# Kernel tuning notes

Hardware: AMD Instinct MI355X
Metric: run time of the kernel (lower is better)

## Reference

```python
import jax, jax.numpy as jnp
import numpy as np

N_NODES = 100000
N_EDGES = 1600000
NFEAT, NHID1, NCLASS = 256, 128, 64
NUM_GRAPHS = 64


def gcn_conv(x, edge_index, edge_weight, W, b):
    # PyG GCNConv: linear transform, add self-loops (weight 1), symmetric norm, scatter-add
    n = x.shape[0]
    x = x @ W  # [N, out]
    loop = jnp.arange(n)
    row = jnp.concatenate([edge_index[0], loop])  # source
    col = jnp.concatenate([edge_index[1], loop])  # target
    w = jnp.concatenate([edge_weight, jnp.ones((n,), dtype=x.dtype)])
    deg = jax.ops.segment_sum(w, col, num_segments=n)
    dinv = jnp.where(deg > 0, jax.lax.rsqrt(jnp.maximum(deg, 1e-30)), 0.0)
    norm = dinv[row] * w * dinv[col]  # [E+N]
    out = jax.ops.segment_sum(x[row] * norm[:, None], col, num_segments=n)
    return out + b


def setup_inputs() -> dict:
    key = jax.random.key(0)
    ks = jax.random.split(key, 12)
    x = jax.random.normal(ks[0], (N_NODES, NFEAT), dtype=jnp.float32)
    edge_index = jax.random.randint(ks[1], (2, N_EDGES), 0, N_NODES, dtype=jnp.int64)
    edge_weight = jax.random.uniform(ks[2], (N_EDGES,), dtype=jnp.float32)
    batch = jnp.sort(jax.random.randint(ks[3], (N_NODES,), 0, NUM_GRAPHS, dtype=jnp.int64))
    def glorot(k, shape):
        lim = float(np.sqrt(6.0 / (shape[0] + shape[1])))
        return jax.random.uniform(k, shape, jnp.float32, -lim, lim)
    W1 = glorot(ks[4], (NFEAT, NHID1)); b1 = jnp.zeros((NHID1,), jnp.float32)
    W2 = glorot(ks[5], (NHID1, NCLASS)); b2 = jnp.zeros((NCLASS,), jnp.float32)
    l1w = glorot(ks[6], (NCLASS, 64)); l1b = jnp.zeros((64,), jnp.float32)
    l2w = glorot(ks[7], (64, 2)); l2b = jnp.zeros((2,), jnp.float32)
    return {"x": x, "edge_index": edge_index, "edge_weight": edge_weight, "batch": batch,
            "W1": W1, "b1": b1, "W2": W2, "b2": b2,
            "l1w": l1w, "l1b": l1b, "l2w": l2w, "l2b": l2b}


def reference(x, edge_index, edge_weight, batch, W1, b1, W2, b2, l1w, l1b, l2w, l2b):
    h = jax.nn.relu(gcn_conv(x, edge_index, edge_weight, W1, b1))
    h = jax.nn.relu(gcn_conv(h, edge_index, edge_weight, W2, b2))
    pooled = jax.ops.segment_sum(h, batch, num_segments=NUM_GRAPHS)  # global_add_pool
    h = jax.nn.relu(pooled @ l1w + l1b)
    out = h @ l2w + l2b
    Y_prob = jax.nn.log_softmax(out, axis=1)
    Y_hat = jnp.argmax(Y_prob, axis=1).astype(jnp.float32)
    return (Y_prob, Y_hat, out)
```

## Files before the change

### kernel.cpp

```cpp
#include <hip/hip_runtime.h>
#include <hip/hip_bf16.h>
#include <math.h>

#define N_NODES 100000
#define N_EDGES 1600000
#define NFEAT 256
#define NHID1 128
#define NCLASS 64
#define NUM_GRAPHS 64

#define NBUCK 391
#define EPB 8192
#define NBLK_A 196

typedef __attribute__((ext_vector_type(8))) short bf16x8;
typedef __attribute__((ext_vector_type(4))) float f32x4;
typedef __attribute__((ext_vector_type(4))) unsigned u32x4;


__device__ __forceinline__ unsigned short f2bf(float f) {
    unsigned u = __float_as_uint(f);
    u += 0x7fffu + ((u >> 16) & 1u);
    return (unsigned short)(u >> 16);
}
__device__ __forceinline__ unsigned packbf2(float lo, float hi) {
    return (unsigned)f2bf(lo) | ((unsigned)f2bf(hi) << 16);
}
__device__ __forceinline__ float bflo(unsigned p) { return __uint_as_float(p << 16); }
__device__ __forceinline__ float bfhi(unsigned p) { return __uint_as_float(p & 0xffff0000u); }


__global__ __launch_bounds__(256) void hist_kernel(const int* __restrict__ cols,
                                                   int* __restrict__ ghist, int nE) {
    __shared__ int h[NBUCK];
    const int tid = threadIdx.x;
    for (int i = tid; i < NBUCK; i += 256) h[i] = 0;
    __syncthreads();
    long base = (long)blockIdx.x * EPB;
    for (int j = tid; j < EPB; j += 256) {
        long idx = base + j;
        if (idx < nE) atomicAdd(&h[cols[idx] >> 8], 1);
    }
    __syncthreads();
    for (int i = tid; i < NBUCK; i += 256) {
        int v = h[i];
        if (v) atomicAdd(&ghist[i], v);
    }
}


__global__ __launch_bounds__(512) void bucket_scan_kernel(const int* __restrict__ ghist,
                                                          int* __restrict__ gbase,
                                                          int* __restrict__ gcursor) {
    __shared__ int sh[512];
    int t = threadIdx.x;
    int v = (t < NBUCK) ? ghist[t] : 0;
    sh[t] = v;
    __syncthreads();
    for (int off = 1; off < 512; off <<= 1) {
        int add = (t >= off) ? sh[t - off] : 0;
        __syncthreads();
        sh[t] += add;
        __syncthreads();
    }
    if (t < NBUCK) {
        int excl = sh[t] - v;
        gbase[t] = excl;
        gcursor[t] = excl;
    }
}


__global__ __launch_bounds__(256) void scatter_bucket_kernel(const int* __restrict__ rows,
                                                             const int* __restrict__ cols,
                                                             const float* __restrict__ w,
                                                             int* __restrict__ gcursor,
                                                             int2* __restrict__ csc_tmp, int nE) {
    __shared__ int h[NBUCK];
    __shared__ int bb[NBUCK];
    __shared__ unsigned short rk[EPB];
    const int tid = threadIdx.x;
    for (int i = tid; i < NBUCK; i += 256) h[i] = 0;
    __syncthreads();
    long base = (long)blockIdx.x * EPB;
    for (int j = tid; j < EPB; j += 256) {
        long idx = base + j;
        if (idx < nE) rk[j] = (unsigned short)atomicAdd(&h[cols[idx] >> 8], 1);
    }
    __syncthreads();
    for (int i = tid; i < NBUCK; i += 256) {
        int v = h[i];
        if (v) bb[i] = atomicAdd(&gcursor[i], v);
    }
    __syncthreads();
    for (int j = tid; j < EPB; j += 256) {
        long idx = base + j;
        if (idx < nE) {
            int c = cols[idx];
            int b = c >> 8;
            int pos = bb[b] + (int)rk[j];
            csc_tmp[pos] = make_int2((rows[idx] & 0x1FFFF) | ((c & 255) << 17),
                                     __float_as_int(w[idx]));
        }
    }
}


__global__ __launch_bounds__(256) void build_csc_kernel(const int2* __restrict__ csc_tmp,
                                                        const int* __restrict__ gbase,
                                                        const int* __restrict__ ghist,
                                                        int2* __restrict__ edges,
                                                        int* __restrict__ starts,
                                                        int* __restrict__ cnt,
                                                        float* __restrict__ dinv, int n) {
    __shared__ int ncnt[256];
    __shared__ float nws[256];
    __shared__ int sh[256];
    __shared__ int ncur[256];
    const int tid = threadIdx.x;
    const int b = blockIdx.x;
    const int base = gbase[b];
    const int cntb = ghist[b];

    ncnt[tid] = 0;
    nws[tid] = 0.f;
    __syncthreads();

    for (int i = tid; i < cntb; i += 256) {
        int2 rec = csc_tmp[base + i];
        int local = ((unsigned)rec.x) >> 17;
        atomicAdd(&ncnt[local], 1);
        atomicAdd(&nws[local], __int_as_float(rec.y));
    }
    __syncthreads();

    int v = ncnt[tid];
    sh[tid] = v;
    __syncthreads();
    for (int off = 1; off < 256; off <<= 1) {
        int add = (tid >= off) ? sh[tid - off] : 0;
        __syncthreads();
        sh[tid] += add;
        __syncthreads();
    }
    int excl = sh[tid] - v;
    ncur[tid] = excl;

    int node = (b << 8) + tid;
    if (node < n) {
        cnt[node] = v;
        starts[node] = base + excl;
        dinv[node] = rsqrtf(1.0f + nws[tid]);
    }
    __syncthreads();

    for (int i = tid; i < cntb; i += 256) {
        int2 rec = csc_tmp[base + i];
        int local = ((unsigned)rec.x) >> 17;
        int r = rec.x & 0x1FFFF;
        int pos = base + atomicAdd(&ncur[local], 1);
        edges[pos] = make_int2(r, rec.y);
    }
}


__global__ void transpose_bf_kernel(const float* __restrict__ W, unsigned* __restrict__ WT,
                                    int K, int Nn) {
    int idx = blockIdx.x * blockDim.x + threadIdx.x;
    int total = Nn * (K / 2);
    if (idx < total) {
        int n = idx / (K / 2);
        int kp = idx - n * (K / 2);
        WT[idx] = packbf2(W[(2 * kp) * Nn + n], W[(2 * kp + 1) * Nn + n]);
    }
}


template <int NT, int KK, bool ABF16>
__global__ __launch_bounds__(256) void gemm_mfma(const void* __restrict__ Av,
                                                 const unsigned* __restrict__ BT,
                                                 const float* __restrict__ rowscale,
                                                 unsigned short* __restrict__ C,
                                                 int M) {
    constexpr int CT = NT / 16;
    constexpr int KD = KK / 2;
    __shared__ unsigned Al[4][128][4];
    __shared__ unsigned Bl[4][NT][4];
    const int tid = threadIdx.x;
    const int wave = tid >> 6;
    const int lane = tid & 63;
    const int quad = lane >> 4;
    const int l16 = lane & 15;
    const int row0 = blockIdx.x * 128;

    f32x4 acc[2][CT] = {};

    for (int k0 = 0; k0 < KK; k0 += 32) {
        if (ABF16) {
            const unsigned* Ab = (const unsigned*)Av;
            #pragma unroll
            for (int i = 0; i < 2; i++) {
                int idx = tid + i * 256;
                int ar = idx >> 2, aq = idx & 3;
                uint4 v = make_uint4(0, 0, 0, 0);
                if (row0 + ar < M)
                    v = *(const uint4*)(Ab + (long)(row0 + ar) * KD + k0 / 2 + aq * 4);
                *(uint4*)&Al[aq][ar][0] = v;
            }
        } else {
            const float* Af = (const float*)Av;
            int ar = tid >> 1, ah = tid & 1;
            float4 v0 = make_float4(0, 0, 0, 0), v1 = v0, v2 = v0, v3 = v0;
            if (row0 + ar < M) {
                const float* p = Af + (long)(row0 + ar) * KK + k0 + ah * 16;
                v0 = *(const float4*)p;
                v1 = *(const float4*)(p + 4);
                v2 = *(const float4*)(p + 8);
                v3 = *(const float4*)(p + 12);
            }
            uint4 d0 = make_uint4(packbf2(v0.x, v0.y), packbf2(v0.z, v0.w),
                                  packbf2(v1.x, v1.y), packbf2(v1.z, v1.w));
            uint4 d1 = make_uint4(packbf2(v2.x, v2.y), packbf2(v2.z, v2.w),
                                  packbf2(v3.x, v3.y), packbf2(v3.z, v3.w));
            *(uint4*)&Al[ah * 2 + 0][ar][0] = d0;
            *(uint4*)&Al[ah * 2 + 1][ar][0] = d1;
        }
        #pragma unroll
        for (int i = 0; i < NT / 64; i++) {
            int idx = tid + i * 256;
            int br = idx >> 2, bq = idx & 3;
            *(uint4*)&Bl[bq][br][0] = *(const uint4*)(BT + (long)br * KD + k0 / 2 + bq * 4);
        }
        __syncthreads();

        bf16x8 af[2];
        #pragma unroll
        for (int rt = 0; rt < 2; rt++)
            af[rt] = *(const bf16x8*)&Al[quad][wave * 32 + rt * 16 + l16][0];
        #pragma unroll
        for (int ct = 0; ct < CT; ct++) {
            bf16x8 bfr = *(const bf16x8*)&Bl[quad][ct * 16 + l16][0];
            acc[0][ct] = __builtin_amdgcn_mfma_f32_16x16x32_bf16(af[0], bfr, acc[0][ct], 0, 0, 0);
            acc[1][ct] = __builtin_amdgcn_mfma_f32_16x16x32_bf16(af[1], bfr, acc[1][ct], 0, 0, 0);
        }
        __syncthreads();
    }

    #pragma unroll
    for (int rt = 0; rt < 2; rt++) {
        #pragma unroll
        for (int reg = 0; reg < 4; reg++) {
            int row = row0 + wave * 32 + rt * 16 + quad * 4 + reg;
            if (row < M) {
                float sc = rowscale[row];
                unsigned short* cp = C + (long)row * NT + l16;
                #pragma unroll
                for (int ct = 0; ct < CT; ct++)
                    cp[ct * 16] = f2bf(acc[rt][ct][reg] * sc);
            }
        }
    }
}


template <int F, bool RELU, int OUTMODE>
__global__ __launch_bounds__(256) void gather_agg_bf(const unsigned* __restrict__ xsb,
                                                     const int2* __restrict__ edges,
                                                     const int* __restrict__ starts,
                                                     const int* __restrict__ cnt,
                                                     const float* __restrict__ dinv,
                                                     const float* __restrict__ bias,
                                                     const int* __restrict__ batch,
                                                     void* __restrict__ outv, int n) {
    constexpr int G = F / 8;
    constexpr int FU = F / 2;
    int gt = blockIdx.x * blockDim.x + threadIdx.x;
    int node = gt / G;
    int lane = gt - node * G;

    if (OUTMODE != 2 && node >= n) return;
    bool active = (node < n);

    __shared__ float lp[4][64];
    int g0 = 0;
    if (OUTMODE == 2) {
        lp[threadIdx.x >> 6][threadIdx.x & 63] = 0.f;
        int firstnode = (blockIdx.x * blockDim.x) / G;
        if (firstnode >= n) firstnode = n - 1;
        g0 = batch[firstnode];
        __syncthreads();
    }

    float acc[8] = {};
    float d = 0.f;
    const unsigned* lbase = xsb + lane * 4;

    if (active) {
        int s = starts[node];
        int c = cnt[node];
        int e = s + c;

        int j = s;
        for (; j + 3 < e; j += 4) {
            long long q0 = __builtin_nontemporal_load((const long long*)(edges + j));
            long long q1 = __builtin_nontemporal_load((const long long*)(edges + j + 1));
            long long q2 = __builtin_nontemporal_load((const long long*)(edges + j + 2));
            long long q3 = __builtin_nontemporal_load((const long long*)(edges + j + 3));
            int r0 = (int)q0, r1 = (int)q1, r2 = (int)q2, r3 = (int)q3;
            float w0 = __int_as_float((int)(q0 >> 32));
            float w1 = __int_as_float((int)(q1 >> 32));
            float w2 = __int_as_float((int)(q2 >> 32));
            float w3 = __int_as_float((int)(q3 >> 32));
            uint4 p0 = *(const uint4*)(lbase + (long)r0 * FU);
            uint4 p1 = *(const uint4*)(lbase + (long)r1 * FU);
            uint4 p2 = *(const uint4*)(lbase + (long)r2 * FU);
            uint4 p3 = *(const uint4*)(lbase + (long)r3 * FU);
            acc[0] += bflo(p0.x) * w0; acc[1] += bfhi(p0.x) * w0;
            acc[2] += bflo(p0.y) * w0; acc[3] += bfhi(p0.y) * w0;
            acc[4] += bflo(p0.z) * w0; acc[5] += bfhi(p0.z) * w0;
            acc[6] += bflo(p0.w) * w0; acc[7] += bfhi(p0.w) * w0;
            acc[0] += bflo(p1.x) * w1; acc[1] += bfhi(p1.x) * w1;
            acc[2] += bflo(p1.y) * w1; acc[3] += bfhi(p1.y) * w1;
            acc[4] += bflo(p1.z) * w1; acc[5] += bfhi(p1.z) * w1;
            acc[6] += bflo(p1.w) * w1; acc[7] += bfhi(p1.w) * w1;
            acc[0] += bflo(p2.x) * w2; acc[1] += bfhi(p2.x) * w2;
            acc[2] += bflo(p2.y) * w2; acc[3] += bfhi(p2.y) * w2;
            acc[4] += bflo(p2.z) * w2; acc[5] += bfhi(p2.z) * w2;
            acc[6] += bflo(p2.w) * w2; acc[7] += bfhi(p2.w) * w2;
            acc[0] += bflo(p3.x) * w3; acc[1] += bfhi(p3.x) * w3;
            acc[2] += bflo(p3.y) * w3; acc[3] += bfhi(p3.y) * w3;
            acc[4] += bflo(p3.z) * w3; acc[5] += bfhi(p3.z) * w3;
            acc[6] += bflo(p3.w) * w3; acc[7] += bfhi(p3.w) * w3;
        }
        for (; j < e; j++) {
            long long q = __builtin_nontemporal_load((const long long*)(edges + j));
            int r = (int)q;
            float wv = __int_as_float((int)(q >> 32));
            uint4 p = *(const uint4*)(lbase + (long)r * FU);
            acc[0] += bflo(p.x) * wv; acc[1] += bfhi(p.x) * wv;
            acc[2] += bflo(p.y) * wv; acc[3] += bfhi(p.y) * wv;
            acc[4] += bflo(p.z) * wv; acc[5] += bfhi(p.z) * wv;
            acc[6] += bflo(p.w) * wv; acc[7] += bfhi(p.w) * wv;
        }
        d = dinv[node];
    }

    float r[8] = {};
    if (active) {
        uint4 sp = *(const uint4*)(lbase + (long)node * FU);
        float sv[8] = { bflo(sp.x), bfhi(sp.x), bflo(sp.y), bfhi(sp.y),
                        bflo(sp.z), bfhi(sp.z), bflo(sp.w), bfhi(sp.w) };
        float4 bb0 = ((const float4*)bias)[lane * 2];
        float4 bb1 = ((const float4*)bias)[lane * 2 + 1];
        float bbv[8] = { bb0.x, bb0.y, bb0.z, bb0.w, bb1.x, bb1.y, bb1.z, bb1.w };
        #pragma unroll
        for (int i = 0; i < 8; i++) {
            float v = d * (acc[i] + sv[i]) + bbv[i];
            r[i] = RELU ? fmaxf(v, 0.f) : v;
        }
    }

    if (OUTMODE == 1) {
        if (active) {
            unsigned* ob = (unsigned*)outv;
            u32x4 pk = { packbf2(r[0], r[1]), packbf2(r[2], r[3]),
                         packbf2(r[4], r[5]), packbf2(r[6], r[7]) };
            __builtin_nontemporal_store(pk, (u32x4*)(ob + (long)node * FU + lane * 4));
        }
    } else if (OUTMODE == 0) {
        if (active) {
            float* o = (float*)outv + (long)node * F + lane * 8;
            *(float4*)o       = make_float4(r[0], r[1], r[2], r[3]);
            *(float4*)(o + 4) = make_float4(r[4], r[5], r[6], r[7]);
        }
    } else {
        float* pooled = (float*)outv;
        if (active) {
            int g = batch[node];
            int rel = g - g0;
            if (rel >= 0 && rel < 4) {
                #pragma unroll
                for (int i = 0; i < 8; i++)
                    atomicAdd(&lp[rel][lane * 8 + i], r[i]);
            } else {
                #pragma unroll
                for (int i = 0; i < 8; i++)
                    atomicAdd(&pooled[g * 64 + lane * 8 + i], r[i]);
            }
        }
        __syncthreads();
        int idx = threadIdx.x;
        int rel = idx >> 6, feat = idx & 63;
        float v = lp[rel][feat];
        int g = g0 + rel;
        if (v != 0.f && g < NUM_GRAPHS)
            atomicAdd(&pooled[g * 64 + feat], v);
    }
}


__global__ __launch_bounds__(256) void head_kernel(const float* __restrict__ pooled,
                                                   const float* __restrict__ l1w,
                                                   const float* __restrict__ l1b,
                                                   const float* __restrict__ l2w,
                                                   const float* __restrict__ l2b,
                                                   float* __restrict__ out) {
    __shared__ float P[64][68];
    __shared__ float W[64][68];
    __shared__ float red0[64][4];
    __shared__ float red1[64][4];
    const int tid = threadIdx.x;

    for (int i = tid; i < 1024; i += 256) {
        int r = i >> 4;
        int cq = (i & 15) * 4;
        *(float4*)&P[r][cq] = *(const float4*)&pooled[r * 64 + cq];
        *(float4*)&W[r][cq] = *(const float4*)&l1w[r * 64 + cq];
    }
    __syncthreads();

    const int g = tid >> 2;
    const int q = tid & 3;
    const int j0 = q * 16;

    float hacc[16];
    #pragma unroll
    for (int jj = 0; jj < 16; jj++) hacc[jj] = l1b[j0 + jj];

    for (int c = 0; c < 64; c++) {
        float pv = P[g][c];
        #pragma unroll
        for (int jj = 0; jj < 16; jj += 4) {
            float4 wv = *(const float4*)&W[c][j0 + jj];
            hacc[jj + 0] += pv * wv.x;
            hacc[jj + 1] += pv * wv.y;
            hacc[jj + 2] += pv * wv.z;
            hacc[jj + 3] += pv * wv.w;
        }
    }

    float o0 = 0.f, o1 = 0.f;
    #pragma unroll
    for (int jj = 0; jj < 16; jj++) {
        float h = fmaxf(hacc[jj], 0.f);
        o0 += h * l2w[(j0 + jj) * 2];
        o1 += h * l2w[(j0 + jj) * 2 + 1];
    }
    red0[g][q] = o0;
    red1[g][q] = o1;
    __syncthreads();

    if (q == 0) {
        float a0 = red0[g][0] + red0[g][1] + red0[g][2] + red0[g][3] + l2b[0];
        float a1 = red1[g][0] + red1[g][1] + red1[g][2] + red1[g][3] + l2b[1];
        float m = fmaxf(a0, a1);
        float lse = m + logf(expf(a0 - m) + expf(a1 - m));
        out[g * 2 + 0] = a0 - lse;
        out[g * 2 + 1] = a1 - lse;
        out[128 + g] = (a1 > a0) ? 1.f : 0.f;
        out[192 + g * 2 + 0] = a0;
        out[192 + g * 2 + 1] = a1;
    }
}


extern "C" void kernel_launch(void* const* d_in, const int* in_sizes, int n_in,
                              void* d_out, int out_size, void* d_ws, size_t ws_size,
                              hipStream_t stream) {
    const float* x   = (const float*)d_in[0];
    const int* eidx  = (const int*)d_in[1];
    const float* ew  = (const float*)d_in[2];
    const int* batch = (const int*)d_in[3];
    const float* W1  = (const float*)d_in[4];
    const float* b1  = (const float*)d_in[5];
    const float* W2  = (const float*)d_in[6];
    const float* b2  = (const float*)d_in[7];
    const float* l1w = (const float*)d_in[8];
    const float* l1b = (const float*)d_in[9];
    const float* l2w = (const float*)d_in[10];
    const float* l2b = (const float*)d_in[11];
    float* out = (float*)d_out;

    const int N = N_NODES, E = N_EDGES;
    const int* rows = eidx;
    const int* cols = eidx + E;

    float* ws = (float*)d_ws;
    int*   ghist   = (int*)ws;
    int*   gbase   = ghist + 512;
    int*   gcursor = gbase + 512;
    float* dinv    = (float*)(gcursor + 512);
    int*   cnt     = (int*)(dinv + N);
    int*   starts  = cnt + N;
    unsigned* w1t  = (unsigned*)(starts + N);
    unsigned* w2t  = w1t + 16384;
    int2*  csc_tmp = (int2*)(w2t + 4096);
    int2*  edges   = csc_tmp + E;
    unsigned* xsb  = (unsigned*)(edges + E);
    unsigned* h1b  = xsb + (long)N * 64;
    float* pooled  = (float*)(h1b + (long)N * 64);
    unsigned* hw2b = xsb;

    hipMemsetAsync(ghist, 0, 512 * sizeof(int), stream);
    hist_kernel<<<NBLK_A, 256, 0, stream>>>(cols, ghist, E);

    bucket_scan_kernel<<<1, 512, 0, stream>>>(ghist, gbase, gcursor);

    scatter_bucket_kernel<<<NBLK_A, 256, 0, stream>>>(rows, cols, ew, gcursor, csc_tmp, E);

    build_csc_kernel<<<NBUCK, 256, 0, stream>>>(csc_tmp, gbase, ghist, edges, starts, cnt, dinv, N);

    transpose_bf_kernel<<<64, 256, 0, stream>>>(W1, w1t, NFEAT, NHID1);
    transpose_bf_kernel<<<16, 256, 0, stream>>>(W2, w2t, NHID1, NCLASS);

    gemm_mfma<NHID1, NFEAT, false><<<(N + 127) / 128, 256, 0, stream>>>(
        x, w1t, dinv, (unsigned short*)xsb, N);

    {
        long threads = (long)N * (NHID1 / 8);
        gather_agg_bf<NHID1, true, 1><<<(threads + 255) / 256, 256, 0, stream>>>(
            xsb, edges, starts, cnt, dinv, b1, batch, h1b, N);
    }

    gemm_mfma<NCLASS, NHID1, true><<<(N + 127) / 128, 256, 0, stream>>>(
        h1b, w2t, dinv, (unsigned short*)hw2b, N);

    hipMemsetAsync(pooled, 0, NUM_GRAPHS * NCLASS * sizeof(float), stream);
    {
        long threads = (long)N * (NCLASS / 8);
        gather_agg_bf<NCLASS, true, 2><<<(threads + 255) / 256, 256, 0, stream>>>(
            hw2b, edges, starts, cnt, dinv, b2, batch, pooled, N);
    }

    head_kernel<<<1, 256, 0, stream>>>(pooled, l1w, l1b, l2w, l2b, out);
}
```

Before: 436.4 us.

## Restructure GEMM to stream A from registers, stage C via LDS, merge transposes

The GEMM now loads A fragments straight from global memory into registers and stages half of B in LDS per pass. This removes the per-32-K-step LDS round trip and the paired barriers. Output tiles are written into LDS first and then stored with coalesced 16-byte writes instead of scattered 2-byte stores. The two weight-transpose launches are merged into one kernel, and the gather kernel drops its nontemporal loads and stores in favour of plain accesses. In exchange, A rows are read with less coalescing, and LDS use and register pressure rise.

```diff
diff --git a/kernel.cpp b/kernel.cpp
--- a/kernel.cpp
+++ b/kernel.cpp
@@ -15,7 +15,6 @@
 
 typedef __attribute__((ext_vector_type(8))) short bf16x8;
 typedef __attribute__((ext_vector_type(4))) float f32x4;
-typedef __attribute__((ext_vector_type(4))) unsigned u32x4;
 
 
 __device__ __forceinline__ unsigned short f2bf(float f) {
@@ -164,14 +163,16 @@
 }
 
 
-__global__ void transpose_bf_kernel(const float* __restrict__ W, unsigned* __restrict__ WT,
-                                    int K, int Nn) {
+__global__ void transpose2_kernel(const float* __restrict__ W1, unsigned* __restrict__ W1T,
+                                  const float* __restrict__ W2, unsigned* __restrict__ W2T) {
     int idx = blockIdx.x * blockDim.x + threadIdx.x;
-    int total = Nn * (K / 2);
-    if (idx < total) {
-        int n = idx / (K / 2);
-        int kp = idx - n * (K / 2);
-        WT[idx] = packbf2(W[(2 * kp) * Nn + n], W[(2 * kp + 1) * Nn + n]);
+    if (idx < 16384) {
+        int n = idx >> 7, kp = idx & 127;
+        W1T[idx] = packbf2(W1[(2 * kp) * NHID1 + n], W1[(2 * kp + 1) * NHID1 + n]);
+    } else if (idx < 16384 + 4096) {
+        int i2 = idx - 16384;
+        int n = i2 >> 6, kp = i2 & 63;
+        W2T[i2] = packbf2(W2[(2 * kp) * NCLASS + n], W2[(2 * kp + 1) * NCLASS + n]);
     }
 }
 
@@ -184,80 +185,95 @@
                                                  int M) {
     constexpr int CT = NT / 16;
     constexpr int KD = KK / 2;
-    __shared__ unsigned Al[4][128][4];
-    __shared__ unsigned Bl[4][NT][4];
+    constexpr int BHP = KD / 2 + 4;
+    constexpr int BSZ = NT * BHP * 4;
+    constexpr int CPITCH = NT + 8;
+    constexpr int CSZ = 128 * CPITCH * 2;
+    constexpr int SMEM = (BSZ > CSZ) ? BSZ : CSZ;
+    __shared__ __align__(16) unsigned char smem[SMEM];
+    unsigned* Bl = reinterpret_cast<unsigned*>(smem);
+    unsigned short* Cl = reinterpret_cast<unsigned short*>(smem);
+
     const int tid = threadIdx.x;
     const int wave = tid >> 6;
     const int lane = tid & 63;
     const int quad = lane >> 4;
     const int l16 = lane & 15;
     const int row0 = blockIdx.x * 128;
+    const int arow0 = row0 + wave * 32 + l16;
 
     f32x4 acc[2][CT] = {};
 
-    for (int k0 = 0; k0 < KK; k0 += 32) {
-        if (ABF16) {
-            const unsigned* Ab = (const unsigned*)Av;
+    #pragma unroll
+    for (int h = 0; h < 2; h++) {
+        if (h) __syncthreads();
+        for (int i = tid; i < NT * (KD / 8); i += 256) {
+            int br = i / (KD / 8);
+            int bq = i - br * (KD / 8);
+            *(uint4*)&Bl[br * BHP + bq * 4] =
+                *(const uint4*)(BT + (long)br * KD + h * (KD / 2) + bq * 4);
+        }
+        __syncthreads();
+
+        #pragma unroll
+        for (int kl = 0; kl < KK / 64; kl++) {
+            const int ki = h * (KK / 64) + kl;
+            bf16x8 af[2];
             #pragma unroll
-            for (int i = 0; i < 2; i++) {
-                int idx = tid + i * 256;
-                int ar = idx >> 2, aq = idx & 3;
+            for (int rt = 0; rt < 2; rt++) {
+                int r = arow0 + rt * 16;
                 uint4 v = make_uint4(0, 0, 0, 0);
-                if (row0 + ar < M)
-                    v = *(const uint4*)(Ab + (long)(row0 + ar) * KD + k0 / 2 + aq * 4);
-                *(uint4*)&Al[aq][ar][0] = v;
+                if (ABF16) {
+                    const unsigned* Ab = (const unsigned*)Av;
+                    if (r < M)
+                        v = *(const uint4*)(Ab + (long)r * KD + ki * 16 + quad * 4);
+                } else {
+                    const float* Af = (const float*)Av;
+                    float4 a0 = make_float4(0, 0, 0, 0), a1 = a0;
+                    if (r < M) {
+                        const float* p = Af + (long)r * KK + ki * 32 + quad * 8;
+                        a0 = *(const float4*)p;
+                        a1 = *(const float4*)(p + 4);
+                    }
+                    v = make_uint4(packbf2(a0.x, a0.y), packbf2(a0.z, a0.w),
+                                   packbf2(a1.x, a1.y), packbf2(a1.z, a1.w));
+                }
+                af[rt] = *reinterpret_cast<bf16x8*>(&v);
             }
-        } else {
-            const float* Af = (const float*)Av;
-            int ar = tid >> 1, ah = tid & 1;
-            float4 v0 = make_float4(0, 0, 0, 0), v1 = v0, v2 = v0, v3 = v0;
-            if (row0 + ar < M) {
-                const float* p = Af + (long)(row0 + ar) * KK + k0 + ah * 16;
-                v0 = *(const float4*)p;
-                v1 = *(const float4*)(p + 4);
-                v2 = *(const float4*)(p + 8);
-                v3 = *(const float4*)(p + 12);
+            #pragma unroll
+            for (int ct = 0; ct < CT; ct++) {
+                bf16x8 bfr = *(const bf16x8*)&Bl[(ct * 16 + l16) * BHP + kl * 16 + quad * 4];
+                acc[0][ct] = __builtin_amdgcn_mfma_f32_16x16x32_bf16(af[0], bfr, acc[0][ct], 0, 0, 0);
+                acc[1][ct] = __builtin_amdgcn_mfma_f32_16x16x32_bf16(af[1], bfr, acc[1][ct], 0, 0, 0);
             }
-            uint4 d0 = make_uint4(packbf2(v0.x, v0.y), packbf2(v0.z, v0.w),
-                                  packbf2(v1.x, v1.y), packbf2(v1.z, v1.w));
-            uint4 d1 = make_uint4(packbf2(v2.x, v2.y), packbf2(v2.z, v2.w),
-                                  packbf2(v3.x, v3.y), packbf2(v3.z, v3.w));
-            *(uint4*)&Al[ah * 2 + 0][ar][0] = d0;
-            *(uint4*)&Al[ah * 2 + 1][ar][0] = d1;
-        }
-        #pragma unroll
-        for (int i = 0; i < NT / 64; i++) {
-            int idx = tid + i * 256;
-            int br = idx >> 2, bq = idx & 3;
-            *(uint4*)&Bl[bq][br][0] = *(const uint4*)(BT + (long)br * KD + k0 / 2 + bq * 4);
-        }
-        __syncthreads();
-
-        bf16x8 af[2];
-        #pragma unroll
-        for (int rt = 0; rt < 2; rt++)
-            af[rt] = *(const bf16x8*)&Al[quad][wave * 32 + rt * 16 + l16][0];
-        #pragma unroll
-        for (int ct = 0; ct < CT; ct++) {
-            bf16x8 bfr = *(const bf16x8*)&Bl[quad][ct * 16 + l16][0];
-            acc[0][ct] = __builtin_amdgcn_mfma_f32_16x16x32_bf16(af[0], bfr, acc[0][ct], 0, 0, 0);
-            acc[1][ct] = __builtin_amdgcn_mfma_f32_16x16x32_bf16(af[1], bfr, acc[1][ct], 0, 0, 0);
-        }
-        __syncthreads();
-    }
+        }
+    }
+    __syncthreads();
 
     #pragma unroll
     for (int rt = 0; rt < 2; rt++) {
         #pragma unroll
         for (int reg = 0; reg < 4; reg++) {
-            int row = row0 + wave * 32 + rt * 16 + quad * 4 + reg;
-            if (row < M) {
-                float sc = rowscale[row];
-                unsigned short* cp = C + (long)row * NT + l16;
-                #pragma unroll
-                for (int ct = 0; ct < CT; ct++)
-                    cp[ct * 16] = f2bf(acc[rt][ct][reg] * sc);
-            }
+            int rl = wave * 32 + rt * 16 + quad * 4 + reg;
+            int grow = row0 + rl;
+            float sc = (grow < M) ? rowscale[grow] : 0.f;
+            unsigned short* cp = Cl + rl * CPITCH + l16;
+            #pragma unroll
+            for (int ct = 0; ct < CT; ct++)
+                cp[ct * 16] = f2bf(acc[rt][ct][reg] * sc);
+        }
+    }
+    __syncthreads();
+
+    constexpr int RDW = NT / 2;
+    unsigned* Cg = (unsigned*)C;
+    for (int i = tid * 4; i < 128 * RDW; i += 256 * 4) {
+        int r = i / RDW;
+        int c = i - r * RDW;
+        int grow = row0 + r;
+        if (grow < M) {
+            uint4 v = *(const uint4*)(Cl + r * CPITCH + c * 2);
+            *(uint4*)(Cg + (long)grow * RDW + c) = v;
         }
     }
 }
@@ -294,6 +310,7 @@
     float acc[8] = {};
     float d = 0.f;
     const unsigned* lbase = xsb + lane * 4;
+    float r[8] = {};
 
     if (active) {
         int s = starts[node];
@@ -302,19 +319,18 @@
 
         int j = s;
         for (; j + 3 < e; j += 4) {
-            long long q0 = __builtin_nontemporal_load((const long long*)(edges + j));
-            long long q1 = __builtin_nontemporal_load((const long long*)(edges + j + 1));
-            long long q2 = __builtin_nontemporal_load((const long long*)(edges + j + 2));
-            long long q3 = __builtin_nontemporal_load((const long long*)(edges + j + 3));
-            int r0 = (int)q0, r1 = (int)q1, r2 = (int)q2, r3 = (int)q3;
-            float w0 = __int_as_float((int)(q0 >> 32));
-            float w1 = __int_as_float((int)(q1 >> 32));
-            float w2 = __int_as_float((int)(q2 >> 32));
-            float w3 = __int_as_float((int)(q3 >> 32));
-            uint4 p0 = *(const uint4*)(lbase + (long)r0 * FU);
-            uint4 p1 = *(const uint4*)(lbase + (long)r1 * FU);
-            uint4 p2 = *(const uint4*)(lbase + (long)r2 * FU);
-            uint4 p3 = *(const uint4*)(lbase + (long)r3 * FU);
+            int2 e0 = edges[j];
+            int2 e1 = edges[j + 1];
+            int2 e2 = edges[j + 2];
+            int2 e3 = edges[j + 3];
+            uint4 p0 = *(const uint4*)(lbase + (long)e0.x * FU);
+            uint4 p1 = *(const uint4*)(lbase + (long)e1.x * FU);
+            uint4 p2 = *(const uint4*)(lbase + (long)e2.x * FU);
+            uint4 p3 = *(const uint4*)(lbase + (long)e3.x * FU);
+            float w0 = __int_as_float(e0.y);
+            float w1 = __int_as_float(e1.y);
+            float w2 = __int_as_float(e2.y);
+            float w3 = __int_as_float(e3.y);
             acc[0] += bflo(p0.x) * w0; acc[1] += bfhi(p0.x) * w0;
             acc[2] += bflo(p0.y) * w0; acc[3] += bfhi(p0.y) * w0;
             acc[4] += bflo(p0.z) * w0; acc[5] += bfhi(p0.z) * w0;
@@ -333,20 +349,16 @@
             acc[6] += bflo(p3.w) * w3; acc[7] += bfhi(p3.w) * w3;
         }
         for (; j < e; j++) {
-            long long q = __builtin_nontemporal_load((const long long*)(edges + j));
-            int r = (int)q;
-            float wv = __int_as_float((int)(q >> 32));
-            uint4 p = *(const uint4*)(lbase + (long)r * FU);
+            int2 ed = edges[j];
+            float wv = __int_as_float(ed.y);
+            uint4 p = *(const uint4*)(lbase + (long)ed.x * FU);
             acc[0] += bflo(p.x) * wv; acc[1] += bfhi(p.x) * wv;
             acc[2] += bflo(p.y) * wv; acc[3] += bfhi(p.y) * wv;
             acc[4] += bflo(p.z) * wv; acc[5] += bfhi(p.z) * wv;
             acc[6] += bflo(p.w) * wv; acc[7] += bfhi(p.w) * wv;
         }
+
         d = dinv[node];
-    }
-
-    float r[8] = {};
-    if (active) {
         uint4 sp = *(const uint4*)(lbase + (long)node * FU);
         float sv[8] = { bflo(sp.x), bfhi(sp.x), bflo(sp.y), bfhi(sp.y),
                         bflo(sp.z), bfhi(sp.z), bflo(sp.w), bfhi(sp.w) };
@@ -363,9 +375,9 @@
     if (OUTMODE == 1) {
         if (active) {
             unsigned* ob = (unsigned*)outv;
-            u32x4 pk = { packbf2(r[0], r[1]), packbf2(r[2], r[3]),
-                         packbf2(r[4], r[5]), packbf2(r[6], r[7]) };
-            __builtin_nontemporal_store(pk, (u32x4*)(ob + (long)node * FU + lane * 4));
+            uint4 pk = make_uint4(packbf2(r[0], r[1]), packbf2(r[2], r[3]),
+                                  packbf2(r[4], r[5]), packbf2(r[6], r[7]));
+            *(uint4*)(ob + (long)node * FU + lane * 4) = pk;
         }
     } else if (OUTMODE == 0) {
         if (active) {
@@ -510,8 +522,7 @@
 
     build_csc_kernel<<<NBUCK, 256, 0, stream>>>(csc_tmp, gbase, ghist, edges, starts, cnt, dinv, N);
 
-    transpose_bf_kernel<<<64, 256, 0, stream>>>(W1, w1t, NFEAT, NHID1);
-    transpose_bf_kernel<<<16, 256, 0, stream>>>(W2, w2t, NHID1, NCLASS);
+    transpose2_kernel<<<80, 256, 0, stream>>>(W1, w1t, W2, w2t);
 
     gemm_mfma<NHID1, NFEAT, false><<<(N + 127) / 128, 256, 0, stream>>>(
         x, w1t, dinv, (unsigned short*)xsb, N);
```

After: 420.9 us. 3.6% less time.
